# Performance work log

Hardware: AMD Instinct MI355X
Metric: run time of the kernel (lower is better)

## Reference

```python
import jax, jax.numpy as jnp
import numpy as np

NEG_BIG = -2.0**32 + 1.0  # padding value used by the torch module


def setup_inputs() -> dict:
    key = jax.random.key(0)
    k1, k2, k3, k4 = jax.random.split(key, 4)
    B, T, D = 8, 1024, 1024
    x = jax.random.normal(k1, (B, T, D), dtype=jnp.float32)
    mask = jnp.ones((B, T), dtype=jnp.float32)
    Wq = jax.random.normal(k2, (D, D), dtype=jnp.float32) * 0.02
    Wk = jax.random.normal(k3, (D, D), dtype=jnp.float32) * 0.02
    Wv = jax.random.normal(k4, (D, D), dtype=jnp.float32) * 0.02
    return {"x": x, "mask": mask, "Wq": Wq, "Wk": Wk, "Wv": Wv}


def reference(x, mask, Wq, Wk, Wv):
    # direction = FORWARD, dropout = 0.0, n_heads = 8
    n_heads = 8
    B, T, D = x.shape
    d = D // n_heads

    # nn.Linear(bias=False): y = x @ W.T
    Q = x @ Wq.T
    K = x @ Wk.T
    V = x @ Wv.T

    # torch.cat(torch.split(Q, d, dim=2), dim=0) -> [h*B, T, d], head-major
    def heads(t):
        return t.reshape(B, T, n_heads, d).transpose(2, 0, 1, 3)  # (h,B,T,d)

    Qh, Kh, Vh = heads(Q), heads(K), heads(V)

    scores = jnp.einsum('hbqd,hbkd->hbqk', Qh, Kh) / jnp.sqrt(jnp.float32(d))

    # key padding mask from K_ itself
    key_masks = jnp.sign(jnp.sum(jnp.abs(Kh), axis=-1))  # (h,B,T)
    scores = jnp.where(key_masks[:, :, None, :] == 0, jnp.float32(NEG_BIG), scores)

    # FORWARD direction: sw_col[i,j]=i, sw_row[i,j]=j; mask = (j > i) -> strict upper tri
    dir_mask = jnp.triu(jnp.ones((T, T), dtype=jnp.float32), k=1)
    adder = (1.0 - dir_mask) * -10000.0
    scores = scores + adder  # broadcasts over (h,B)

    attn = jax.nn.softmax(scores, axis=-1)

    query_masks = jnp.sign(jnp.sum(jnp.abs(Qh), axis=-1))  # (h,B,T)
    attn = attn * query_masks[:, :, :, None]

    out = jnp.einsum('hbqk,hbkd->hbqd', attn, Vh)  # (h,B,T,d)
    out = out.transpose(1, 2, 0, 3).reshape(B, T, D)  # cat heads back on feature dim

    out = out * mask[:, :, None]
    return out
```

## Files before the change

### kernel.cpp

```cpp
#include <hip/hip_runtime.h>
#include <hip/hip_bf16.h>
#include <stdint.h>


typedef __attribute__((ext_vector_type(8))) short short8;
typedef __attribute__((ext_vector_type(4))) float floatx4;

__device__ __forceinline__ short f2bf(float f) {
    union { float f; uint32_t u; } v; v.f = f;
    uint32_t r = v.u + 0x7fffu + ((v.u >> 16) & 1u);
    return (short)(r >> 16);
}
__device__ __forceinline__ float bf2f(short u) {
    union { float f; uint32_t x; } v; v.x = ((uint32_t)(uint16_t)u) << 16;
    return v.f;
}

__device__ __forceinline__ void load_lds_16B(const void* g, void* l) {
    __builtin_amdgcn_global_load_lds(
        (const __attribute__((address_space(1))) void*)g,
        (__attribute__((address_space(3))) void*)l, 16, 0, 0);
}

__global__ __launch_bounds__(256) void cast_all_kernel(
    const float* __restrict__ x, const float* __restrict__ w0,
    const float* __restrict__ w1, const float* __restrict__ w2,
    short* __restrict__ xb, short* __restrict__ wb)
{
    int bid = blockIdx.x;
    const float* src;
    short* dst;
    int i;
    if (bid < 4096) {
        src = x; dst = xb; i = bid * 256 + threadIdx.x;
    } else {
        int sel = (bid - 4096) >> 9;
        int blk = (bid - 4096) & 511;
        src = (sel == 0) ? w0 : ((sel == 1) ? w1 : w2);
        dst = wb + sel * 1048576;
        i = blk * 256 + threadIdx.x;
    }
    float4 a = *(const float4*)(src + i * 8);
    float4 b = *(const float4*)(src + i * 8 + 4);
    short8 o;
    o[0] = f2bf(a.x); o[1] = f2bf(a.y); o[2] = f2bf(a.z); o[3] = f2bf(a.w);
    o[4] = f2bf(b.x); o[5] = f2bf(b.y); o[6] = f2bf(b.z); o[7] = f2bf(b.w);
    *(short8*)(dst + i * 8) = o;
}

__global__ __launch_bounds__(256) void qkv_gemm_kernel(
    const short* __restrict__ xb, const short* __restrict__ wb,
    short* __restrict__ Qh, short* __restrict__ Kh, short* __restrict__ VhT)
{
    __shared__ short As[2][4096];
    __shared__ short Bs[2][4096];
    __shared__ short Cs[8704];

    const int tid = threadIdx.x;
    const int m0 = blockIdx.x * 128;
    const int n0 = blockIdx.y * 128;
    const int wave = tid >> 6;
    const int lane = tid & 63;
    const int wm = (wave >> 1) * 64;
    const int wn = (wave & 1) * 64;
    const int l16 = lane & 15;
    const int quad = lane >> 4;
    const int srow = lane >> 2;
    const int scol = (lane & 3) * 8;

    floatx4 zero = {0.0f, 0.0f, 0.0f, 0.0f};
    floatx4 acc[4][4];
    for (int i = 0; i < 4; ++i)
        for (int j = 0; j < 4; ++j) acc[i][j] = zero;

    auto stage = [&](int k0, int bf) {
        #pragma unroll
        for (int c = 0; c < 4; ++c) {
            int chunk = wave * 4 + c;
            if (chunk < 8)
                load_lds_16B(xb + (m0 + chunk * 16 + srow) * 1024 + k0 + scol,
                             &As[bf][chunk * 512]);
            else
                load_lds_16B(wb + (n0 + (chunk - 8) * 16 + srow) * 1024 + k0 + scol,
                             &Bs[bf][(chunk - 8) * 512]);
        }
    };

    stage(0, 0);
    int buf = 0;
    for (int k0 = 0; k0 < 1024; k0 += 32) {
        __syncthreads();
        if (k0 + 32 < 1024) stage(k0 + 32, buf ^ 1);

        short8 a[4], b[4];
        #pragma unroll
        for (int i = 0; i < 4; ++i)
            a[i] = *(const short8*)&As[buf][(wm + i * 16 + l16) * 32 + quad * 8];
        #pragma unroll
        for (int j = 0; j < 4; ++j)
            b[j] = *(const short8*)&Bs[buf][(wn + j * 16 + l16) * 32 + quad * 8];
        #pragma unroll
        for (int i = 0; i < 4; ++i)
            #pragma unroll
            for (int j = 0; j < 4; ++j)
                acc[i][j] = __builtin_amdgcn_mfma_f32_16x16x32_bf16(a[i], b[j], acc[i][j], 0, 0, 0);
        buf ^= 1;
    }

    const float qscale = 0.08838834764831845f;
    const int f0 = n0 & 1023;
    const int h = f0 >> 7;
    const bool isV = (n0 >= 2048);
    const float sc = (n0 < 1024) ? qscale : 1.0f;
    short* dst = (n0 < 1024) ? Qh : Kh;

    #pragma unroll
    for (int half = 0; half < 2; ++half) {
        __syncthreads();
        if ((wave >> 1) == half) {
            #pragma unroll
            for (int i = 0; i < 4; ++i)
                #pragma unroll
                for (int j = 0; j < 4; ++j)
                    #pragma unroll
                    for (int p = 0; p < 4; ++p) {
                        int mr = i * 16 + quad * 4 + p;
                        int c = wn + j * 16 + l16;
                        short v = f2bf(acc[i][j][p] * sc);
                        if (isV) Cs[c * 68 + mr] = v;
                        else     Cs[mr * 132 + c] = v;
                    }
        }
        __syncthreads();
        if (!isV) {
            #pragma unroll
            for (int jj = 0; jj < 4; ++jj) {
                int idx = tid + jj * 256;
                int row = idx >> 4;
                int chunk = idx & 15;
                int m = m0 + half * 64 + row;
                int bb = m >> 10, t = m & 1023;
                *(short8*)&dst[((h * 8 + bb) * 1024 + t) * 128 + chunk * 8] =
                    *(const short8*)&Cs[row * 132 + chunk * 8];
            }
        } else {
            int m = m0 + half * 64;
            int bb = m >> 10, t = m & 1023;
            #pragma unroll
            for (int jj = 0; jj < 4; ++jj) {
                int idx = tid + jj * 256;
                int dd = idx >> 3;
                int chunk = idx & 7;
                *(short8*)&VhT[((h * 8 + bb) * 128 + dd) * 1024 + t + chunk * 8] =
                    *(const short8*)&Cs[dd * 68 + chunk * 8];
            }
        }
    }
}

#define LDP 70

__global__ __launch_bounds__(256) void attn_kernel(
    const short* __restrict__ Qh, const short* __restrict__ Kh,
    const short* __restrict__ VhT, const float* __restrict__ mask,
    float* __restrict__ out)
{
    __shared__ short Kb[2][8192];
    __shared__ short Vb[2][8192];
    __shared__ short Ps[4 * 16 * LDP];

    const int tid = threadIdx.x;
    const int hb = blockIdx.x;
    const int qt = blockIdx.y;
    const int h = hb >> 3, b = hb & 7;

    const int wave = tid >> 6;
    const int lane = tid & 63;
    const int l16 = lane & 15;
    const int quad = lane >> 4;

    const int base = hb * 131072;
    const short* Qp = Qh + base;
    const short* Kp = Kh + base;
    const short* VTp = VhT + base;
    short* Pw = &Ps[wave * 16 * LDP];

    const int q0_lo = qt * 64 + wave * 16;
    const int q0_hi = (15 - qt) * 64 + wave * 16;
    const int hi_start = 15 - qt;

    short8 aq_lo[4], aq_hi[4];
    #pragma unroll
    for (int kk = 0; kk < 4; ++kk) {
        aq_lo[kk] = *(const short8*)(Qp + (q0_lo + l16) * 128 + kk * 32 + quad * 8);
        aq_hi[kk] = *(const short8*)(Qp + (q0_hi + l16) * 128 + kk * 32 + quad * 8);
    }

    floatx4 zero = {0.0f, 0.0f, 0.0f, 0.0f};
    floatx4 o_lo[8], o_hi[8];
    #pragma unroll
    for (int n = 0; n < 8; ++n) { o_lo[n] = zero; o_hi[n] = zero; }
    float l_lo[4] = {0, 0, 0, 0}, l_hi[4] = {0, 0, 0, 0};

    auto stage = [&](int kt, int bf) {
        #pragma unroll
        for (int c = 0; c < 4; ++c) {
            int L = wave * 4 + c;
            int kk = L >> 2, rg = L & 3;
            load_lds_16B(Kp + (kt * 64 + rg * 16 + (lane >> 2)) * 128 + kk * 32 + (lane & 3) * 8,
                         &Kb[bf][kk * 2048 + rg * 512]);
        }
        #pragma unroll
        for (int c = 0; c < 4; ++c) {
            int L = wave * 4 + c;
            int kk2 = L >> 3, g = L & 7;
            load_lds_16B(VTp + (g * 16 + (lane >> 2)) * 1024 + kt * 64 + kk2 * 32 + (lane & 3) * 8,
                         &Vb[bf][kk2 * 4096 + g * 512]);
        }
    };

    auto s_phase = [&](int bf, const short8* aq, floatx4* s) {
        #pragma unroll
        for (int sub = 0; sub < 4; ++sub) {
            s[sub] = zero;
            #pragma unroll
            for (int kk = 0; kk < 4; ++kk) {
                short8 bk = *(const short8*)&Kb[bf][kk * 2048 + (sub * 16 + l16) * 32 + quad * 8];
                s[sub] = __builtin_amdgcn_mfma_f32_16x16x32_bf16(aq[kk], bk, s[sub], 0, 0, 0);
            }
        }
    };
    auto exp_phase = [&](floatx4* s, int q0g, float* l, int kt) {
        #pragma unroll
        for (int sub = 0; sub < 4; ++sub)
            #pragma unroll
            for (int p = 0; p < 4; ++p) {
                int qg = q0g + quad * 4 + p;
                int kg = kt * 64 + sub * 16 + l16;
                float sv = s[sub][p];
                if (kg <= qg && qg != 1023) sv -= 10000.0f;
                float e = __expf(sv);
                l[p] += e;
                Pw[(quad * 4 + p) * LDP + sub * 16 + l16] = f2bf(e);
            }
    };
    auto pv_phase = [&](int bf, floatx4* o) {
        #pragma unroll
        for (int kk2 = 0; kk2 < 2; ++kk2) {
            short8 ap = *(const short8*)&Pw[l16 * LDP + kk2 * 32 + quad * 8];
            #pragma unroll
            for (int n = 0; n < 8; ++n) {
                short8 bv = *(const short8*)&Vb[bf][kk2 * 4096 + (n * 16 + l16) * 32 + quad * 8];
                o[n] = __builtin_amdgcn_mfma_f32_16x16x32_bf16(ap, bv, o[n], 0, 0, 0);
            }
        }
    };

    stage(qt, 0);
    int buf = 0;
    for (int kt = qt; kt < 16; ++kt) {
        __syncthreads();
        if (kt + 1 < 16) stage(kt + 1, buf ^ 1);
        const bool do_hi = (kt >= hi_start);
        floatx4 s_lo[4], s_hi[4];
        s_phase(buf, aq_lo, s_lo);
        exp_phase(s_lo, q0_lo, l_lo, kt);
        if (do_hi) s_phase(buf, aq_hi, s_hi);
        pv_phase(buf, o_lo);
        if (do_hi) {
            exp_phase(s_hi, q0_hi, l_hi, kt);
            pv_phase(buf, o_hi);
        }
        buf ^= 1;
    }

    #pragma unroll
    for (int off = 8; off >= 1; off >>= 1)
        #pragma unroll
        for (int p = 0; p < 4; ++p) {
            l_lo[p] += __shfl_xor(l_lo[p], off);
            l_hi[p] += __shfl_xor(l_hi[p], off);
        }

    #pragma unroll
    for (int p = 0; p < 4; ++p) {
        int qg = q0_lo + quad * 4 + p;
        float s = (1.0f / l_lo[p]) * mask[b * 1024 + qg];
        #pragma unroll
        for (int n = 0; n < 8; ++n)
            out[(b * 1024 + qg) * 1024 + h * 128 + n * 16 + l16] = o_lo[n][p] * s;
    }
    #pragma unroll
    for (int p = 0; p < 4; ++p) {
        int qg = q0_hi + quad * 4 + p;
        float s = (1.0f / l_hi[p]) * mask[b * 1024 + qg];
        #pragma unroll
        for (int n = 0; n < 8; ++n)
            out[(b * 1024 + qg) * 1024 + h * 128 + n * 16 + l16] = o_hi[n][p] * s;
    }
}

__global__ __launch_bounds__(256) void row1023_kernel(
    const short* __restrict__ Qh, const short* __restrict__ Kh,
    const short* __restrict__ VhT, const float* __restrict__ mask,
    float* __restrict__ out)
{
    __shared__ float qv[128];
    __shared__ float ps[1024];
    __shared__ float red[4];

    const int hb = blockIdx.x;
    const int h = hb >> 3, b = hb & 7;
    const int base = hb * 131072;
    const int tid = threadIdx.x;
    const int wave = tid >> 6, lane = tid & 63;

    if (tid < 128) qv[tid] = bf2f(Qh[base + 1023 * 128 + tid]);
    __syncthreads();

    float tot = 0.0f;
    #pragma unroll
    for (int kk = 0; kk < 4; ++kk) {
        int k = tid * 4 + kk;
        const short8* kr = (const short8*)(Kh + base + k * 128);
        float acc = 0.0f;
        #pragma unroll
        for (int c = 0; c < 16; ++c) {
            short8 v = kr[c];
            #pragma unroll
            for (int j = 0; j < 8; ++j) acc += qv[c * 8 + j] * bf2f(v[j]);
        }
        float e = __expf(acc);
        ps[k] = e;
        tot += e;
    }
    #pragma unroll
    for (int off = 32; off >= 1; off >>= 1) tot += __shfl_xor(tot, off);
    if (lane == 0) red[wave] = tot;
    __syncthreads();
    float inv = 1.0f / (red[0] + red[1] + red[2] + red[3]);
    inv *= mask[b * 1024 + 1023];

    int dd = tid >> 1, half = tid & 1;
    const short* vr = VhT + base + dd * 1024 + half * 512;
    const float* pp = ps + half * 512;
    float acc = 0.0f;
    for (int k = 0; k < 512; k += 8) {
        short8 v = *(const short8*)(vr + k);
        #pragma unroll
        for (int j = 0; j < 8; ++j) acc += pp[k + j] * bf2f(v[j]);
    }
    acc += __shfl_xor(acc, 1);
    if (half == 0)
        out[(b * 1024 + 1023) * 1024 + h * 128 + dd] = acc * inv;
}

extern "C" void kernel_launch(void* const* d_in, const int* in_sizes, int n_in,
                              void* d_out, int out_size, void* d_ws, size_t ws_size,
                              hipStream_t stream) {
    const float* x    = (const float*)d_in[0];
    const float* mask = (const float*)d_in[1];
    const float* Wq   = (const float*)d_in[2];
    const float* Wk   = (const float*)d_in[3];
    const float* Wv   = (const float*)d_in[4];
    float* out = (float*)d_out;

    short* xb  = (short*)d_ws;
    short* wb  = xb + 8388608;
    short* Qh  = wb + 3145728;
    short* Kh  = Qh + 8388608;
    short* VhT = Kh + 8388608;

    cast_all_kernel<<<5632, 256, 0, stream>>>(x, Wq, Wk, Wv, xb, wb);
    qkv_gemm_kernel<<<dim3(64, 24), 256, 0, stream>>>(xb, wb, Qh, Kh, VhT);
    attn_kernel<<<dim3(64, 8), 256, 0, stream>>>(Qh, Kh, VhT, mask, out);
    row1023_kernel<<<64, 256, 0, stream>>>(Qh, Kh, VhT, mask, out);
}
```

Before: 247.2 us.

## Swizzle LDS tiles, alias GEMM epilogue buffer, fold row-1023 kernel into attention

Applies an XOR swizzle to the 16-byte column chunks written to and read from LDS in the QKV GEMM and attention kernels, aiming to cut LDS bank conflicts on MFMA operand reads. The GEMM's C staging buffer now aliases the A/B buffers, which shrinks LDS use and may allow more blocks per CU. The separate row-1023 kernel becomes an extra blockIdx.y slice of the attention grid, removing one launch and letting that work run alongside the main attention blocks. The hi-tile store now skips row 1023 so it does not race with the special block.

```diff
diff --git a/kernel.cpp b/kernel.cpp
--- a/kernel.cpp
+++ b/kernel.cpp
@@ -52,9 +52,10 @@
     const short* __restrict__ xb, const short* __restrict__ wb,
     short* __restrict__ Qh, short* __restrict__ Kh, short* __restrict__ VhT)
 {
-    __shared__ short As[2][4096];
-    __shared__ short Bs[2][4096];
-    __shared__ short Cs[8704];
+    __shared__ short smem[16384];
+    short* As = smem;
+    short* Bs = smem + 8192;
+    short* Cs = smem;
 
     const int tid = threadIdx.x;
     const int m0 = blockIdx.x * 128;
@@ -66,7 +67,8 @@
     const int l16 = lane & 15;
     const int quad = lane >> 4;
     const int srow = lane >> 2;
-    const int scol = (lane & 3) * 8;
+    const int scb = ((lane & 3) ^ ((lane >> 3) & 3)) * 8;
+    const int rq  = (quad ^ ((l16 >> 1) & 3)) * 8;
 
     floatx4 zero = {0.0f, 0.0f, 0.0f, 0.0f};
     floatx4 acc[4][4];
@@ -78,11 +80,11 @@
         for (int c = 0; c < 4; ++c) {
             int chunk = wave * 4 + c;
             if (chunk < 8)
-                load_lds_16B(xb + (m0 + chunk * 16 + srow) * 1024 + k0 + scol,
-                             &As[bf][chunk * 512]);
+                load_lds_16B(xb + (m0 + chunk * 16 + srow) * 1024 + k0 + scb,
+                             &As[bf * 4096 + chunk * 512]);
             else
-                load_lds_16B(wb + (n0 + (chunk - 8) * 16 + srow) * 1024 + k0 + scol,
-                             &Bs[bf][(chunk - 8) * 512]);
+                load_lds_16B(wb + (n0 + (chunk - 8) * 16 + srow) * 1024 + k0 + scb,
+                             &Bs[bf * 4096 + (chunk - 8) * 512]);
         }
     };
 
@@ -95,10 +97,10 @@
         short8 a[4], b[4];
         #pragma unroll
         for (int i = 0; i < 4; ++i)
-            a[i] = *(const short8*)&As[buf][(wm + i * 16 + l16) * 32 + quad * 8];
+            a[i] = *(const short8*)&As[buf * 4096 + (wm + i * 16 + l16) * 32 + rq];
         #pragma unroll
         for (int j = 0; j < 4; ++j)
-            b[j] = *(const short8*)&Bs[buf][(wn + j * 16 + l16) * 32 + quad * 8];
+            b[j] = *(const short8*)&Bs[buf * 4096 + (wn + j * 16 + l16) * 32 + rq];
         #pragma unroll
         for (int i = 0; i < 4; ++i)
             #pragma unroll
@@ -173,13 +175,63 @@
     const int hb = blockIdx.x;
     const int qt = blockIdx.y;
     const int h = hb >> 3, b = hb & 7;
+    const int base = hb * 131072;
+
+    if (qt == 8) {
+        float* qv = (float*)&Kb[0][0];
+        float* ps = qv + 128;
+        float* red = ps + 1024;
+        const int wave = tid >> 6, lane = tid & 63;
+
+        if (tid < 128) qv[tid] = bf2f(Qh[base + 1023 * 128 + tid]);
+        __syncthreads();
+
+        float tot = 0.0f;
+        #pragma unroll
+        for (int kk = 0; kk < 4; ++kk) {
+            int k = tid * 4 + kk;
+            const short8* kr = (const short8*)(Kh + base + k * 128);
+            float acc = 0.0f;
+            #pragma unroll
+            for (int c = 0; c < 16; ++c) {
+                short8 v = kr[c];
+                #pragma unroll
+                for (int j = 0; j < 8; ++j) acc += qv[c * 8 + j] * bf2f(v[j]);
+            }
+            float e = __expf(acc);
+            ps[k] = e;
+            tot += e;
+        }
+        #pragma unroll
+        for (int off = 32; off >= 1; off >>= 1) tot += __shfl_xor(tot, off);
+        if (lane == 0) red[wave] = tot;
+        __syncthreads();
+        float inv = 1.0f / (red[0] + red[1] + red[2] + red[3]);
+        inv *= mask[b * 1024 + 1023];
+
+        int dd = tid >> 1, half = tid & 1;
+        const short* vr = VhT + base + dd * 1024 + half * 512;
+        const float* pp = ps + half * 512;
+        float acc = 0.0f;
+        for (int k = 0; k < 512; k += 8) {
+            short8 v = *(const short8*)(vr + k);
+            #pragma unroll
+            for (int j = 0; j < 8; ++j) acc += pp[k + j] * bf2f(v[j]);
+        }
+        acc += __shfl_xor(acc, 1);
+        if (half == 0)
+            out[(b * 1024 + 1023) * 1024 + h * 128 + dd] = acc * inv;
+        return;
+    }
 
     const int wave = tid >> 6;
     const int lane = tid & 63;
     const int l16 = lane & 15;
     const int quad = lane >> 4;
-
-    const int base = hb * 131072;
+    const int srow = lane >> 2;
+    const int scb = ((lane & 3) ^ ((lane >> 3) & 3)) * 8;
+    const int rq  = (quad ^ ((l16 >> 1) & 3)) * 8;
+
     const short* Qp = Qh + base;
     const short* Kp = Kh + base;
     const short* VTp = VhT + base;
@@ -207,14 +259,14 @@
         for (int c = 0; c < 4; ++c) {
             int L = wave * 4 + c;
             int kk = L >> 2, rg = L & 3;
-            load_lds_16B(Kp + (kt * 64 + rg * 16 + (lane >> 2)) * 128 + kk * 32 + (lane & 3) * 8,
+            load_lds_16B(Kp + (kt * 64 + rg * 16 + srow) * 128 + kk * 32 + scb,
                          &Kb[bf][kk * 2048 + rg * 512]);
         }
         #pragma unroll
         for (int c = 0; c < 4; ++c) {
             int L = wave * 4 + c;
             int kk2 = L >> 3, g = L & 7;
-            load_lds_16B(VTp + (g * 16 + (lane >> 2)) * 1024 + kt * 64 + kk2 * 32 + (lane & 3) * 8,
+            load_lds_16B(VTp + (g * 16 + srow) * 1024 + kt * 64 + kk2 * 32 + scb,
                          &Vb[bf][kk2 * 4096 + g * 512]);
         }
     };
@@ -225,7 +277,7 @@
             s[sub] = zero;
             #pragma unroll
             for (int kk = 0; kk < 4; ++kk) {
-                short8 bk = *(const short8*)&Kb[bf][kk * 2048 + (sub * 16 + l16) * 32 + quad * 8];
+                short8 bk = *(const short8*)&Kb[bf][kk * 2048 + (sub * 16 + l16) * 32 + rq];
                 s[sub] = __builtin_amdgcn_mfma_f32_16x16x32_bf16(aq[kk], bk, s[sub], 0, 0, 0);
             }
         }
@@ -250,7 +302,7 @@
             short8 ap = *(const short8*)&Pw[l16 * LDP + kk2 * 32 + quad * 8];
             #pragma unroll
             for (int n = 0; n < 8; ++n) {
-                short8 bv = *(const short8*)&Vb[bf][kk2 * 4096 + (n * 16 + l16) * 32 + quad * 8];
+                short8 bv = *(const short8*)&Vb[bf][kk2 * 4096 + (n * 16 + l16) * 32 + rq];
                 o[n] = __builtin_amdgcn_mfma_f32_16x16x32_bf16(ap, bv, o[n], 0, 0, 0);
             }
         }
@@ -293,66 +345,12 @@
     #pragma unroll
     for (int p = 0; p < 4; ++p) {
         int qg = q0_hi + quad * 4 + p;
+        if (qg == 1023) continue;
         float s = (1.0f / l_hi[p]) * mask[b * 1024 + qg];
         #pragma unroll
         for (int n = 0; n < 8; ++n)
             out[(b * 1024 + qg) * 1024 + h * 128 + n * 16 + l16] = o_hi[n][p] * s;
     }
-}
-
-__global__ __launch_bounds__(256) void row1023_kernel(
-    const short* __restrict__ Qh, const short* __restrict__ Kh,
-    const short* __restrict__ VhT, const float* __restrict__ mask,
-    float* __restrict__ out)
-{
-    __shared__ float qv[128];
-    __shared__ float ps[1024];
-    __shared__ float red[4];
-
-    const int hb = blockIdx.x;
-    const int h = hb >> 3, b = hb & 7;
-    const int base = hb * 131072;
-    const int tid = threadIdx.x;
-    const int wave = tid >> 6, lane = tid & 63;
-
-    if (tid < 128) qv[tid] = bf2f(Qh[base + 1023 * 128 + tid]);
-    __syncthreads();
-
-    float tot = 0.0f;
-    #pragma unroll
-    for (int kk = 0; kk < 4; ++kk) {
-        int k = tid * 4 + kk;
-        const short8* kr = (const short8*)(Kh + base + k * 128);
-        float acc = 0.0f;
-        #pragma unroll
-        for (int c = 0; c < 16; ++c) {
-            short8 v = kr[c];
-            #pragma unroll
-            for (int j = 0; j < 8; ++j) acc += qv[c * 8 + j] * bf2f(v[j]);
-        }
-        float e = __expf(acc);
-        ps[k] = e;
-        tot += e;
-    }
-    #pragma unroll
-    for (int off = 32; off >= 1; off >>= 1) tot += __shfl_xor(tot, off);
-    if (lane == 0) red[wave] = tot;
-    __syncthreads();
-    float inv = 1.0f / (red[0] + red[1] + red[2] + red[3]);
-    inv *= mask[b * 1024 + 1023];
-
-    int dd = tid >> 1, half = tid & 1;
-    const short* vr = VhT + base + dd * 1024 + half * 512;
-    const float* pp = ps + half * 512;
-    float acc = 0.0f;
-    for (int k = 0; k < 512; k += 8) {
-        short8 v = *(const short8*)(vr + k);
-        #pragma unroll
-        for (int j = 0; j < 8; ++j) acc += pp[k + j] * bf2f(v[j]);
-    }
-    acc += __shfl_xor(acc, 1);
-    if (half == 0)
-        out[(b * 1024 + 1023) * 1024 + h * 128 + dd] = acc * inv;
 }
 
 extern "C" void kernel_launch(void* const* d_in, const int* in_sizes, int n_in,
@@ -373,6 +371,5 @@
 
     cast_all_kernel<<<5632, 256, 0, stream>>>(x, Wq, Wk, Wv, xb, wb);
     qkv_gemm_kernel<<<dim3(64, 24), 256, 0, stream>>>(xb, wb, Qh, Kh, VhT);
-    attn_kernel<<<dim3(64, 8), 256, 0, stream>>>(Qh, Kh, VhT, mask, out);
-    row1023_kernel<<<64, 256, 0, stream>>>(Qh, Kh, VhT, mask, out);
-}
+    attn_kernel<<<dim3(64, 9), 256, 0, stream>>>(Qh, Kh, VhT, mask, out);
+}
```

New measurement: 238.2 us. -3.6%, faster.
